# Performance work log

Measured on AMD Instinct MI355X. Metric: run time of the kernel, lower is better.

## Reference

```python
import jax, jax.numpy as jnp
import numpy as np

B, N, K, D = 4, 20000, 16, 128


def setup_inputs() -> dict:
    key = jax.random.key(0)
    k1, k2, k3, k4, k5, k6 = jax.random.split(key, 6)
    node_embeddings = jax.random.normal(k1, (B, N, D), dtype=jnp.float32)
    knn_indices = jax.random.randint(k2, (B, N, K), 0, N, dtype=jnp.int32)
    # MLP params: Linear(3D -> D), GELU, Linear(D -> D)
    s1 = 1.0 / np.sqrt(3 * D)
    s2 = 1.0 / np.sqrt(D)
    W1 = jax.random.uniform(k3, (3 * D, D), dtype=jnp.float32, minval=-s1, maxval=s1)
    b1 = jax.random.uniform(k4, (D,), dtype=jnp.float32, minval=-s1, maxval=s1)
    W2 = jax.random.uniform(k5, (D, D), dtype=jnp.float32, minval=-s2, maxval=s2)
    b2 = jax.random.uniform(k6, (D,), dtype=jnp.float32, minval=-s2, maxval=s2)
    return {"node_embeddings": node_embeddings, "knn_indices": knn_indices,
            "W1": W1, "b1": b1, "W2": W2, "b2": b2}


def reference(node_embeddings, knn_indices, W1, b1, W2, b2):
    # gather neighbors: [B, N, K, D]
    neighbors = jnp.take_along_axis(node_embeddings[:, None, :, :],  # [B,1,N,D]
                                    knn_indices[:, :, :, None].astype(jnp.int32),
                                    axis=2)
    neighbor_mean = neighbors.mean(axis=2)  # [B, N, D]
    feats = jnp.concatenate([node_embeddings, neighbor_mean,
                             node_embeddings - neighbor_mean], axis=-1)  # [B,N,3D]
    h = jax.nn.gelu(feats @ W1 + b1, approximate=False)
    update = h @ W2 + b2
    return node_embeddings + update
```

## Files before the change

kernel.cpp:

```cpp
#include <hip/hip_runtime.h>

#define NB      20000
#define BATCH   4
#define KNN     16
#define DD      128
#define MW      136
#define BMG     32
#define NSLOTG  313
#define BMF     64
#define NSLOTF  157

#define PT_ROWS   32
#define PT_TILES  625
#define WL_BYTES  98304
#define XB_BYTES  16384
#define MB_BYTES  8192
#define HB_BYTES  8192
#define PT_LDS    (WL_BYTES + 2*XB_BYTES + 2*MB_BYTES + HB_BYTES)

#if defined(__has_builtin)
#if __has_builtin(__builtin_amdgcn_cvt_pk_f32_fp8)
#define FP8_DEC_BUILTIN 1
#endif
#endif

typedef __attribute__((ext_vector_type(8))) short          bf16x8;
typedef __attribute__((ext_vector_type(4))) float          f32x4;
typedef __attribute__((ext_vector_type(2))) float          f32x2;
typedef __attribute__((ext_vector_type(4))) int            i32x4;
typedef __attribute__((ext_vector_type(2))) int            i32x2;
typedef __attribute__((ext_vector_type(4))) unsigned short u16x4;
typedef __attribute__((ext_vector_type(8))) unsigned short u16x8;

__device__ __forceinline__ unsigned short f2bf(float f) {
    unsigned int u = __float_as_uint(f);
    u += 0x7fffu + ((u >> 16) & 1u);
    return (unsigned short)(u >> 16);
}
__device__ __forceinline__ float bf2f(unsigned short u) {
    return __uint_as_float((unsigned int)u << 16);
}
__device__ __forceinline__ float gelu_fast(float z) {
    float u = z * (0.7978845608028654f + 0.0356774081f * z * z);
    float e = __expf(-2.0f * u);
    return z * __builtin_amdgcn_rcpf(1.0f + e);
}
__device__ __forceinline__ void glds16(const void* g, void* l) {
    __builtin_amdgcn_global_load_lds(
        (const __attribute__((address_space(1))) void*)g,
        (__attribute__((address_space(3))) void*)l, 16, 0, 0);
}
__device__ __forceinline__ void bar_lgkm() {
    asm volatile("s_waitcnt lgkmcnt(0)" ::: "memory");
    __builtin_amdgcn_sched_barrier(0);
    __builtin_amdgcn_s_barrier();
}
__device__ __forceinline__ void bar_full() {
    asm volatile("s_waitcnt vmcnt(0) lgkmcnt(0)" ::: "memory");
    __builtin_amdgcn_sched_barrier(0);
    __builtin_amdgcn_s_barrier();
}
__device__ __forceinline__ unsigned int f32_to_e4m3(float x) {
    unsigned int u   = __float_as_uint(x);
    unsigned int sgn = (u >> 24) & 0x80u;
    float ax = fabsf(x);
    unsigned int em;
    if (ax < 0.015625f) {
        em = (unsigned int)rintf(ax * 512.0f);
    } else {
        unsigned int mag = __float_as_uint(fminf(ax, 448.0f));
        em = ((mag + 0x7FFFFu + ((mag >> 20) & 1u)) >> 20) - 0x3C0u;
    }
    return sgn | em;
}
__device__ __forceinline__ void acc4_fp8(unsigned int w, float* s) {
#if defined(FP8_DEC_BUILTIN)
    f32x2 lo = __builtin_amdgcn_cvt_pk_f32_fp8((int)w, false);
    f32x2 hi = __builtin_amdgcn_cvt_pk_f32_fp8((int)w, true);
    s[0] += lo[0]; s[1] += lo[1]; s[2] += hi[0]; s[3] += hi[1];
#else
    #pragma unroll
    for (int j = 0; j < 4; ++j) {
        unsigned int b  = (w >> (8 * j)) & 0xFFu;
        unsigned int em = b & 0x7Fu;
        float f  = __uint_as_float((em << 20) + 0x3C000000u);
        float fd = (float)em * 0.001953125f;
        f = (em < 8u) ? fd : f;
        f = __uint_as_float(__float_as_uint(f) | ((b & 0x80u) << 24));
        s[j] += f;
    }
#endif
}
__device__ __forceinline__ u16x4 dec4_bf16(unsigned int w) {
    u16x4 o;
#if defined(FP8_DEC_BUILTIN)
    f32x2 lo = __builtin_amdgcn_cvt_pk_f32_fp8((int)w, false);
    f32x2 hi = __builtin_amdgcn_cvt_pk_f32_fp8((int)w, true);
    o[0] = f2bf(lo[0]); o[1] = f2bf(lo[1]); o[2] = f2bf(hi[0]); o[3] = f2bf(hi[1]);
#else
    #pragma unroll
    for (int j = 0; j < 4; ++j) {
        unsigned int b  = (w >> (8 * j)) & 0xFFu;
        unsigned int em = b & 0x7Fu;
        float f  = __uint_as_float((em << 20) + 0x3C000000u);
        float fd = (float)em * 0.001953125f;
        f = (em < 8u) ? fd : f;
        f = __uint_as_float(__float_as_uint(f) | ((b & 0x80u) << 24));
        o[j] = f2bf(f);
    }
#endif
    return o;
}

__device__ __forceinline__ const bf16x8* wfrag(const void* W, int col, int ko) {
    return (const bf16x8*)((const char*)W + col * 256 + (ko ^ ((col & 7) << 4)));
}

__global__ __launch_bounds__(256) void nr_prep(
    const float* __restrict__ emb, const float* __restrict__ W1,
    const float* __restrict__ W2,
    unsigned char* __restrict__ embq, unsigned short* __restrict__ Wsw)
{
    int bid = blockIdx.x;
    if (bid < 5000) {
        long long i = ((long long)bid * 256 + threadIdx.x) * 8;
        const float4* p = (const float4*)(emb + i);
        float4 a = p[0], b = p[1];
        unsigned int w0 = f32_to_e4m3(a.x) | (f32_to_e4m3(a.y) << 8) |
                          (f32_to_e4m3(a.z) << 16) | (f32_to_e4m3(a.w) << 24);
        unsigned int w1 = f32_to_e4m3(b.x) | (f32_to_e4m3(b.y) << 8) |
                          (f32_to_e4m3(b.z) << 16) | (f32_to_e4m3(b.w) << 24);
        i32x2 q; q[0] = (int)w0; q[1] = (int)w1;
        *(i32x2*)(embq + i) = q;
    } else {
        int tid = (bid - 5000) * 256 + threadIdx.x;
        int w   = tid >> 14;
        int r2  = tid & 16383;
        int col = r2 >> 7;
        int k   = r2 & 127;
        float v;
        if (w == 0)      v = W1[k * DD + col] + W1[(256 + k) * DD + col];
        else if (w == 1) v = W1[(128 + k) * DD + col] - W1[(256 + k) * DD + col];
        else             v = W2[k * DD + col];
        char* dst = (char*)Wsw + w * 32768 + col * 256 + ((k * 2) ^ ((col & 7) << 4));
        *(unsigned short*)dst = f2bf(v);
    }
}

__global__ __launch_bounds__(256, 2) void nr_gather(
    const unsigned char* __restrict__ embq, const int* __restrict__ knn,
    unsigned char* __restrict__ meanq)
{
    extern __shared__ char ldsg[];

    const int t     = threadIdx.x;
    const int xcd   = blockIdx.x & 7;
    const int slot  = blockIdx.x >> 3;
    const int batch = xcd >> 1;
    const int bib   = (xcd & 1) * NSLOTG + slot;
    const int mend  = batch * NB + NB;
    int m_base = batch * NB + bib * BMG;
    if (m_base + BMG > mend) m_base = mend - BMG;

    const int node_local = t >> 3;
    const int dpart      = t & 7;
    const int m  = m_base + node_local;
    const int wv = t >> 6;
    const int ln = t & 63;

    int idx[KNN];
    const i32x4* kp4 = (const i32x4*)(knn + (long long)m * KNN);
    #pragma unroll
    for (int q = 0; q < 4; ++q) {
        i32x4 v = __builtin_nontemporal_load(kp4 + q);
        idx[4*q+0] = v[0]; idx[4*q+1] = v[1]; idx[4*q+2] = v[2]; idx[4*q+3] = v[3];
    }

    const unsigned char* qbase = embq + (long long)batch * NB * DD + dpart * 16;
    #pragma unroll
    for (int k = 0; k < KNN; ++k)
        glds16(qbase + (long long)idx[k] * DD, ldsg + k * 4096 + wv * 1024);

    __syncthreads();

    float sm[16];
    #pragma unroll
    for (int e = 0; e < 16; ++e) sm[e] = 0.f;
    #pragma unroll
    for (int k = 0; k < KNN; ++k) {
        i32x4 v = *(const i32x4*)(ldsg + k * 4096 + wv * 1024 + ln * 16);
        acc4_fp8((unsigned int)v[0], sm + 0);
        acc4_fp8((unsigned int)v[1], sm + 4);
        acc4_fp8((unsigned int)v[2], sm + 8);
        acc4_fp8((unsigned int)v[3], sm + 12);
    }

    i32x4 o;
    #pragma unroll
    for (int j = 0; j < 4; ++j) {
        unsigned int w;
        w  = f32_to_e4m3(sm[4*j+0] * 0.0625f);
        w |= f32_to_e4m3(sm[4*j+1] * 0.0625f) << 8;
        w |= f32_to_e4m3(sm[4*j+2] * 0.0625f) << 16;
        w |= f32_to_e4m3(sm[4*j+3] * 0.0625f) << 24;
        o[j] = (int)w;
    }
    *(i32x4*)(meanq + (long long)m * DD + dpart * 16) = o;
}

__global__ __launch_bounds__(512, 2) void nr_persist(
    const float* __restrict__ emb, const unsigned char* __restrict__ meanq,
    const unsigned short* __restrict__ Wsw,
    const float* __restrict__ b1, const float* __restrict__ b2,
    float* __restrict__ out)
{
    extern __shared__ char L[];
    char* WL  = L;
    char* XB0 = L + WL_BYTES;
    char* MB0 = XB0 + 2 * XB_BYTES;
    char* HB  = MB0 + 2 * MB_BYTES;

    const int t     = threadIdx.x;
    const int xcd   = blockIdx.x & 7;
    const int bslot = blockIdx.x >> 3;
    const int batch = xcd >> 1;
    const int pair  = (xcd & 1) * 64 + bslot;
    const int wv    = t >> 6;
    const int ln    = t & 63;
    const int lrow  = ln & 15;
    const int lk    = ln >> 4;
    const int r     = wv & 1;
    const int cf0   = wv >> 1;
    const int arow  = r * 16 + lrow;
    const int xsw   = (arow & 7) << 4;

    int   colj[2]; float b1v[2], b2v[2];
    #pragma unroll
    for (int j = 0; j < 2; ++j) {
        colj[j] = (cf0 + j * 4) * 16 + lrow;
        b1v[j]  = b1[colj[j]];
        b2v[j]  = b2[colj[j]];
    }

    {
        const char* gw = (const char*)Wsw;
        #pragma unroll
        for (int i = 0; i < 12; ++i) {
            int ch = i * 8 + wv;
            glds16(gw + ch * 1024 + ln * 16, WL + ch * 1024);
        }
    }

    const long long brow = (long long)batch * NB;
    const int nt = (PT_TILES - pair + 127) >> 7;

    auto stage_x = [&](int n) {
        const long long r0 = brow + (long long)(pair + n * 128) * PT_ROWS;
        char* xb = XB0 + (n & 1) * XB_BYTES;
        const char* gx = (const char*)emb + r0 * 512;
        #pragma unroll
        for (int ci = 0; ci < 2; ++ci) {
            int ch  = wv * 2 + ci;
            int row = ch * 2 + (ln >> 5);
            int cb  = (ln & 31) * 16;
            glds16(gx + (long long)row * 512 + (cb ^ ((row & 7) << 4)),
                   xb + ch * 1024);
        }
    };
    auto load_mean = [&](int n) -> i32x2 {
        const long long r0 = brow + (long long)(pair + n * 128) * PT_ROWS;
        int row = t >> 4;
        int cb8 = (t & 15) * 8;
        return *(const i32x2*)(meanq + (r0 + row) * 128 + cb8);
    };
    auto write_mean = [&](int n, i32x2 mv) {
        char* mb = MB0 + (n & 1) * MB_BYTES;
        int row = t >> 4;
        int cb8 = (t & 15) * 8;
        u16x4 a = dec4_bf16((unsigned int)mv[0]);
        u16x4 b = dec4_bf16((unsigned int)mv[1]);
        u16x8 o;
        o[0]=a[0]; o[1]=a[1]; o[2]=a[2]; o[3]=a[3];
        o[4]=b[0]; o[5]=b[1]; o[6]=b[2]; o[7]=b[3];
        *(u16x8*)(mb + row * 256 + ((cb8 * 2) ^ ((row & 7) << 4))) = o;
    };

    stage_x(0);
    {
        i32x2 mv0 = load_mean(0);
        write_mean(0, mv0);
    }
    bar_full();

    for (int n = 0; n < nt; ++n) {
        const int p = n & 1;
        char* xb = XB0 + p * XB_BYTES;
        char* mb = MB0 + p * MB_BYTES;
        const long long r0 = brow + (long long)(pair + n * 128) * PT_ROWS;
        const bool have_next = (n + 1 < nt);

        i32x2 mv;
        if (have_next) {
            stage_x(n + 1);
            mv = load_mean(n + 1);
        }

        bf16x8 xf[4], mf[4];
        #pragma unroll
        for (int ks = 0; ks < 4; ++ks) {
            int cb = ks * 128 + lk * 32;
            f32x4 a0 = *(const f32x4*)(xb + arow * 512 + ((cb)      ^ xsw));
            f32x4 a1 = *(const f32x4*)(xb + arow * 512 + ((cb + 16) ^ xsw));
            u16x8 xt;
            xt[0]=f2bf(a0[0]); xt[1]=f2bf(a0[1]); xt[2]=f2bf(a0[2]); xt[3]=f2bf(a0[3]);
            xt[4]=f2bf(a1[0]); xt[5]=f2bf(a1[1]); xt[6]=f2bf(a1[2]); xt[7]=f2bf(a1[3]);
            xf[ks] = *(bf16x8*)&xt;
            mf[ks] = *(const bf16x8*)(mb + arow * 256 + ((ks * 64 + lk * 16) ^ xsw));
        }

        f32x4 acc[2];
        acc[0] = (f32x4){0.f,0.f,0.f,0.f}; acc[1] = (f32x4){0.f,0.f,0.f,0.f};
        #pragma unroll
        for (int ks = 0; ks < 4; ++ks)
            #pragma unroll
            for (int j = 0; j < 2; ++j) {
                bf16x8 w = *wfrag(WL, colj[j], ks * 64 + lk * 16);
                acc[j] = __builtin_amdgcn_mfma_f32_16x16x32_bf16(xf[ks], w, acc[j], 0, 0, 0);
            }
        #pragma unroll
        for (int ks = 0; ks < 4; ++ks)
            #pragma unroll
            for (int j = 0; j < 2; ++j) {
                bf16x8 w = *wfrag(WL + 32768, colj[j], ks * 64 + lk * 16);
                acc[j] = __builtin_amdgcn_mfma_f32_16x16x32_bf16(mf[ks], w, acc[j], 0, 0, 0);
            }

        #pragma unroll
        for (int j = 0; j < 2; ++j)
            #pragma unroll
            for (int rr = 0; rr < 4; ++rr) {
                int row = r * 16 + lk * 4 + rr;
                *(unsigned short*)(HB + row * 256 + ((colj[j] * 2) ^ ((row & 7) << 4)))
                    = f2bf(gelu_fast(acc[j][rr] + b1v[j]));
            }
        bar_lgkm();

        bf16x8 hf[4];
        #pragma unroll
        for (int ks = 0; ks < 4; ++ks)
            hf[ks] = *(const bf16x8*)(HB + arow * 256 + ((ks * 64 + lk * 16) ^ xsw));
        f32x4 acc2[2];
        acc2[0] = (f32x4){0.f,0.f,0.f,0.f}; acc2[1] = (f32x4){0.f,0.f,0.f,0.f};
        #pragma unroll
        for (int ks = 0; ks < 4; ++ks)
            #pragma unroll
            for (int j = 0; j < 2; ++j) {
                bf16x8 w = *wfrag(WL + 65536, colj[j], ks * 64 + lk * 16);
                acc2[j] = __builtin_amdgcn_mfma_f32_16x16x32_bf16(hf[ks], w, acc2[j], 0, 0, 0);
            }

        if (have_next) write_mean(n + 1, mv);

        #pragma unroll
        for (int j = 0; j < 2; ++j)
            #pragma unroll
            for (int rr = 0; rr < 4; ++rr) {
                int row = r * 16 + lk * 4 + rr;
                int col = colj[j];
                float xv = *(const float*)(xb + row * 512 + ((col * 4) ^ ((row & 7) << 4)));
                out[(r0 + row) * 128 + col] = acc2[j][rr] + b2v[j] + xv;
            }
        bar_full();
    }
}

template<int MODE>
__global__ __launch_bounds__(256, 3) void nr_fused(
    const float* __restrict__ emb, const unsigned char* __restrict__ meanq,
    const int* __restrict__ knn, const unsigned short* __restrict__ Wsw,
    const float* __restrict__ b1, const float* __restrict__ b2,
    float* __restrict__ out)
{
    extern __shared__ char ldsraw[];
    float*          ldsxF = (float*)ldsraw;
    unsigned short* ldsm  = (unsigned short*)(ldsraw + BMF * DD * 4);

    const int t     = threadIdx.x;
    const int xcd   = blockIdx.x & 7;
    const int slot  = blockIdx.x >> 3;
    const int batch = xcd >> 1;
    const int bib   = (xcd & 1) * NSLOTF + slot;
    const int mend  = batch * NB + NB;
    int m_base = batch * NB + bib * BMF;
    if (m_base + BMF > mend) m_base = mend - BMF;

    {
        const int node_local = t >> 2;
        const int dpart      = t & 3;
        const int m  = m_base + node_local;
        const int wv = t >> 6;
        const int ln = t & 63;

        if constexpr (MODE == 0) {
            const i32x4* mp = (const i32x4*)(meanq + (long long)m * DD + dpart * 32);
            i32x4 v0 = mp[0], v1 = mp[1];
            const char* gx = (const char*)(emb + (long long)m_base * DD);
            #pragma unroll
            for (int it = 0; it < 8; ++it) {
                int off = it * 4096 + wv * 1024;
                glds16(gx + off + ln * 16, ldsraw + off);
            }
            unsigned short* mrow = ldsm + node_local * MW + dpart * 32;
            #pragma unroll
            for (int j = 0; j < 4; ++j) {
                *(u16x4*)(mrow + j*4)      = dec4_bf16((unsigned int)v0[j]);
                *(u16x4*)(mrow + 16 + j*4) = dec4_bf16((unsigned int)v1[j]);
            }
        } else {
            const f32x4* xp = (const f32x4*)(emb + (long long)m * DD + dpart * 32);
            float* xrow = ldsxF + node_local * DD + dpart * 32;
            #pragma unroll
            for (int j = 0; j < 8; ++j) {
                f32x4 v = xp[j];
                *(f32x4*)(xrow + j*4) = v;
            }
            int idx[KNN];
            const i32x4* kp4 = (const i32x4*)(knn + (long long)m * KNN);
            #pragma unroll
            for (int q = 0; q < 4; ++q) {
                i32x4 v = __builtin_nontemporal_load(kp4 + q);
                idx[4*q+0]=v[0]; idx[4*q+1]=v[1]; idx[4*q+2]=v[2]; idx[4*q+3]=v[3];
            }
            float sm[32];
            #pragma unroll
            for (int e = 0; e < 32; ++e) sm[e] = 0.f;
            const long long bbase = (long long)batch * NB * DD + dpart * 32;
            #pragma unroll 4
            for (int k = 0; k < KNN; ++k) {
                const f32x4* np = (const f32x4*)(emb + bbase + (long long)idx[k] * DD);
                #pragma unroll
                for (int j = 0; j < 8; ++j) {
                    f32x4 v = np[j];
                    sm[j*4+0]+=v[0]; sm[j*4+1]+=v[1]; sm[j*4+2]+=v[2]; sm[j*4+3]+=v[3];
                }
            }
            unsigned short* mrow = ldsm + node_local * MW + dpart * 32;
            #pragma unroll
            for (int j = 0; j < 8; ++j) {
                u16x4 pm;
                #pragma unroll
                for (int e = 0; e < 4; ++e) pm[e] = f2bf(sm[j*4+e] * 0.0625f);
                *(u16x4*)(mrow + j*4) = pm;
            }
        }
    }
    __syncthreads();

    const int wave = t >> 6;
    const int lane = t & 63;
    const int lrow = lane & 15;
    const int lk   = lane >> 4;
    const int Arow = wave * 16 + lrow;

    bf16x8 xf[4], mf[4];
    {
        const float* xr = ldsxF + Arow * DD + lk * 8;
        const unsigned short* mr = ldsm + Arow * MW + lk * 8;
        #pragma unroll
        for (int ks = 0; ks < 4; ++ks) {
            f32x4 a0 = *(const f32x4*)(xr + ks * 32);
            f32x4 a1 = *(const f32x4*)(xr + ks * 32 + 4);
            u16x8 xt;
            xt[0]=f2bf(a0[0]); xt[1]=f2bf(a0[1]); xt[2]=f2bf(a0[2]); xt[3]=f2bf(a0[3]);
            xt[4]=f2bf(a1[0]); xt[5]=f2bf(a1[1]); xt[6]=f2bf(a1[2]); xt[7]=f2bf(a1[3]);
            xf[ks] = *(bf16x8*)&xt;
            mf[ks] = *(const bf16x8*)(mr + ks * 32);
        }
    }

    f32x4 acc[8];
    #pragma unroll
    for (int f = 0; f < 8; ++f) acc[f] = (f32x4){0.f, 0.f, 0.f, 0.f};
    #pragma unroll
    for (int ks = 0; ks < 4; ++ks)
        #pragma unroll
        for (int f = 0; f < 8; ++f) {
            bf16x8 bw = *wfrag(Wsw, f * 16 + lrow, ks * 64 + lk * 16);
            acc[f] = __builtin_amdgcn_mfma_f32_16x16x32_bf16(xf[ks], bw, acc[f], 0, 0, 0);
        }
    #pragma unroll
    for (int ks = 0; ks < 4; ++ks)
        #pragma unroll
        for (int f = 0; f < 8; ++f) {
            bf16x8 bw = *wfrag((const char*)Wsw + 32768, f * 16 + lrow, ks * 64 + lk * 16);
            acc[f] = __builtin_amdgcn_mfma_f32_16x16x32_bf16(mf[ks], bw, acc[f], 0, 0, 0);
        }
    __syncthreads();

    #pragma unroll
    for (int f = 0; f < 8; ++f) {
        int col = f * 16 + lrow;
        float bb = b1[col];
        #pragma unroll
        for (int rr = 0; rr < 4; ++rr) {
            int row = wave * 16 + lk * 4 + rr;
            ldsm[row * MW + col] = f2bf(gelu_fast(acc[f][rr] + bb));
        }
    }
    __syncthreads();

    f32x4 acc2[8];
    #pragma unroll
    for (int f = 0; f < 8; ++f) acc2[f] = (f32x4){0.f, 0.f, 0.f, 0.f};
    {
        const unsigned short* abase = ldsm + Arow * MW + lk * 8;
        #pragma unroll
        for (int ks = 0; ks < 4; ++ks) {
            bf16x8 af = *(const bf16x8*)(abase + ks * 32);
            #pragma unroll
            for (int f = 0; f < 8; ++f) {
                bf16x8 bw = *wfrag((const char*)Wsw + 65536, f * 16 + lrow, ks * 64 + lk * 16);
                acc2[f] = __builtin_amdgcn_mfma_f32_16x16x32_bf16(af, bw, acc2[f], 0, 0, 0);
            }
        }
    }

    #pragma unroll
    for (int f = 0; f < 8; ++f) {
        int col = f * 16 + lrow;
        float bb = b2[col];
        #pragma unroll
        for (int rr = 0; rr < 4; ++rr) {
            int row = wave * 16 + lk * 4 + rr;
            float xv = ldsxF[row * DD + col];
            out[(long long)(m_base + row) * DD + col] = acc2[f][rr] + bb + xv;
        }
    }
}

extern "C" void kernel_launch(void* const* d_in, const int* in_sizes, int n_in,
                              void* d_out, int out_size, void* d_ws, size_t ws_size,
                              hipStream_t stream) {
    const float* emb = (const float*)d_in[0];
    const int*   knn = (const int*)  d_in[1];
    const float* W1  = (const float*)d_in[2];
    const float* b1  = (const float*)d_in[3];
    const float* W2  = (const float*)d_in[4];
    const float* b2  = (const float*)d_in[5];
    float* out = (float*)d_out;

    unsigned short* Wsw   = (unsigned short*)d_ws;
    unsigned char*  embq  = (unsigned char*)(Wsw + 49152);
    unsigned char*  meanq = embq + 10240000;

    const size_t NEED   = (size_t)98304 + 10240000 + 10240000;
    const size_t LDSB_F = (size_t)BMF * DD * 4 + (size_t)BMF * MW * 2;

    if (ws_size >= NEED) {
        hipError_t e = hipFuncSetAttribute(
            reinterpret_cast<const void*>(nr_persist),
            hipFuncAttributeMaxDynamicSharedMemorySize, PT_LDS);
        nr_prep<<<5192, 256, 0, stream>>>(emb, W1, W2, embq, Wsw);
        nr_gather<<<8 * NSLOTG, 256, 65536, stream>>>(embq, knn, meanq);
        if (e == hipSuccess) {
            nr_persist<<<512, 512, PT_LDS, stream>>>(
                emb, meanq, Wsw, b1, b2, out);
        } else {
            nr_fused<0><<<8 * NSLOTF, 256, LDSB_F, stream>>>(
                emb, meanq, knn, Wsw, b1, b2, out);
        }
    } else {
        nr_prep<<<5192, 256, 0, stream>>>(emb, W1, W2, embq, Wsw);
        nr_fused<2><<<8 * NSLOTF, 256, LDSB_F, stream>>>(
            emb, nullptr, knn, Wsw, b1, b2, out);
    }
}
```

Before: 63.71 us.

## Hold weight fragments in registers and halve persistent grid in nr_persist

Moves the three bf16 weight matrices out of LDS into per-thread register fragments loaded once, and loads fp8 mean values straight from global into registers instead of staging them through LDS. LDS use per block drops to the x staging buffers plus the hidden buffer, and the persistent grid goes from 512 to 256 blocks, each handling twice as many tiles. This removes the repeated LDS weight reads in the MFMA loops and the mean staging writes. The cost is higher register pressure from 48 bf16x8 fragments plus prefetched means, which could spill or limit occupancy, and fewer blocks to hide latency. The fallback path is also cleaned up so it no longer needs meanq, and prep skips the emb quantization there.

```diff
diff --git a/kernel.cpp b/kernel.cpp
--- a/kernel.cpp
+++ b/kernel.cpp
@@ -12,11 +12,9 @@
 
 #define PT_ROWS   32
 #define PT_TILES  625
-#define WL_BYTES  98304
 #define XB_BYTES  16384
-#define MB_BYTES  8192
 #define HB_BYTES  8192
-#define PT_LDS    (WL_BYTES + 2*XB_BYTES + 2*MB_BYTES + HB_BYTES)
+#define PT_LDS    (2*XB_BYTES + HB_BYTES)
 
 #if defined(__has_builtin)
 #if __has_builtin(__builtin_amdgcn_cvt_pk_f32_fp8)
@@ -116,13 +114,14 @@
     return (const bf16x8*)((const char*)W + col * 256 + (ko ^ ((col & 7) << 4)));
 }
 
+template<bool DO_EMB>
 __global__ __launch_bounds__(256) void nr_prep(
     const float* __restrict__ emb, const float* __restrict__ W1,
     const float* __restrict__ W2,
     unsigned char* __restrict__ embq, unsigned short* __restrict__ Wsw)
 {
     int bid = blockIdx.x;
-    if (bid < 5000) {
+    if (DO_EMB && bid < 5000) {
         long long i = ((long long)bid * 256 + threadIdx.x) * 8;
         const float4* p = (const float4*)(emb + i);
         float4 a = p[0], b = p[1];
@@ -133,7 +132,7 @@
         i32x2 q; q[0] = (int)w0; q[1] = (int)w1;
         *(i32x2*)(embq + i) = q;
     } else {
-        int tid = (bid - 5000) * 256 + threadIdx.x;
+        int tid = (bid - (DO_EMB ? 5000 : 0)) * 256 + threadIdx.x;
         int w   = tid >> 14;
         int r2  = tid & 16383;
         int col = r2 >> 7;
@@ -215,16 +214,14 @@
     float* __restrict__ out)
 {
     extern __shared__ char L[];
-    char* WL  = L;
-    char* XB0 = L + WL_BYTES;
-    char* MB0 = XB0 + 2 * XB_BYTES;
-    char* HB  = MB0 + 2 * MB_BYTES;
+    char* XB0 = L;
+    char* HB  = L + 2 * XB_BYTES;
 
     const int t     = threadIdx.x;
     const int xcd   = blockIdx.x & 7;
     const int bslot = blockIdx.x >> 3;
     const int batch = xcd >> 1;
-    const int pair  = (xcd & 1) * 64 + bslot;
+    const int pair  = (xcd & 1) * 32 + bslot;
     const int wv    = t >> 6;
     const int ln    = t & 63;
     const int lrow  = ln & 15;
@@ -242,20 +239,22 @@
         b2v[j]  = b2[colj[j]];
     }
 
-    {
-        const char* gw = (const char*)Wsw;
-        #pragma unroll
-        for (int i = 0; i < 12; ++i) {
-            int ch = i * 8 + wv;
-            glds16(gw + ch * 1024 + ln * 16, WL + ch * 1024);
-        }
-    }
+    bf16x8 wA[4][2], wB[4][2], wC[4][2];
+    #pragma unroll
+    for (int ks = 0; ks < 4; ++ks)
+        #pragma unroll
+        for (int j = 0; j < 2; ++j) {
+            int ko = ks * 64 + lk * 16;
+            wA[ks][j] = *wfrag(Wsw, colj[j], ko);
+            wB[ks][j] = *wfrag((const char*)Wsw + 32768, colj[j], ko);
+            wC[ks][j] = *wfrag((const char*)Wsw + 65536, colj[j], ko);
+        }
 
     const long long brow = (long long)batch * NB;
-    const int nt = (PT_TILES - pair + 127) >> 7;
+    const int nt = (PT_TILES - pair + 63) >> 6;
 
     auto stage_x = [&](int n) {
-        const long long r0 = brow + (long long)(pair + n * 128) * PT_ROWS;
+        const long long r0 = brow + (long long)(pair + n * 64) * PT_ROWS;
         char* xb = XB0 + (n & 1) * XB_BYTES;
         const char* gx = (const char*)emb + r0 * 512;
         #pragma unroll
@@ -267,42 +266,28 @@
                    xb + ch * 1024);
         }
     };
-    auto load_mean = [&](int n) -> i32x2 {
-        const long long r0 = brow + (long long)(pair + n * 128) * PT_ROWS;
-        int row = t >> 4;
-        int cb8 = (t & 15) * 8;
-        return *(const i32x2*)(meanq + (r0 + row) * 128 + cb8);
+    auto load_mean = [&](int n, i32x2* mv) {
+        const long long r0 = brow + (long long)(pair + n * 64) * PT_ROWS;
+        const unsigned char* mq = meanq + (r0 + arow) * 128 + lk * 8;
+        #pragma unroll
+        for (int ks = 0; ks < 4; ++ks)
+            mv[ks] = *(const i32x2*)(mq + ks * 32);
     };
-    auto write_mean = [&](int n, i32x2 mv) {
-        char* mb = MB0 + (n & 1) * MB_BYTES;
-        int row = t >> 4;
-        int cb8 = (t & 15) * 8;
-        u16x4 a = dec4_bf16((unsigned int)mv[0]);
-        u16x4 b = dec4_bf16((unsigned int)mv[1]);
-        u16x8 o;
-        o[0]=a[0]; o[1]=a[1]; o[2]=a[2]; o[3]=a[3];
-        o[4]=b[0]; o[5]=b[1]; o[6]=b[2]; o[7]=b[3];
-        *(u16x8*)(mb + row * 256 + ((cb8 * 2) ^ ((row & 7) << 4))) = o;
-    };
-
+
+    i32x2 mv_cur[4], mv_nxt[4];
     stage_x(0);
-    {
-        i32x2 mv0 = load_mean(0);
-        write_mean(0, mv0);
-    }
+    load_mean(0, mv_cur);
     bar_full();
 
     for (int n = 0; n < nt; ++n) {
         const int p = n & 1;
         char* xb = XB0 + p * XB_BYTES;
-        char* mb = MB0 + p * MB_BYTES;
-        const long long r0 = brow + (long long)(pair + n * 128) * PT_ROWS;
+        const long long r0 = brow + (long long)(pair + n * 64) * PT_ROWS;
         const bool have_next = (n + 1 < nt);
 
-        i32x2 mv;
         if (have_next) {
             stage_x(n + 1);
-            mv = load_mean(n + 1);
+            load_mean(n + 1, mv_nxt);
         }
 
         bf16x8 xf[4], mf[4];
@@ -315,7 +300,12 @@
             xt[0]=f2bf(a0[0]); xt[1]=f2bf(a0[1]); xt[2]=f2bf(a0[2]); xt[3]=f2bf(a0[3]);
             xt[4]=f2bf(a1[0]); xt[5]=f2bf(a1[1]); xt[6]=f2bf(a1[2]); xt[7]=f2bf(a1[3]);
             xf[ks] = *(bf16x8*)&xt;
-            mf[ks] = *(const bf16x8*)(mb + arow * 256 + ((ks * 64 + lk * 16) ^ xsw));
+            u16x4 mlo = dec4_bf16((unsigned int)mv_cur[ks][0]);
+            u16x4 mhi = dec4_bf16((unsigned int)mv_cur[ks][1]);
+            u16x8 mt;
+            mt[0]=mlo[0]; mt[1]=mlo[1]; mt[2]=mlo[2]; mt[3]=mlo[3];
+            mt[4]=mhi[0]; mt[5]=mhi[1]; mt[6]=mhi[2]; mt[7]=mhi[3];
+            mf[ks] = *(bf16x8*)&mt;
         }
 
         f32x4 acc[2];
@@ -323,17 +313,13 @@
         #pragma unroll
         for (int ks = 0; ks < 4; ++ks)
             #pragma unroll
-            for (int j = 0; j < 2; ++j) {
-                bf16x8 w = *wfrag(WL, colj[j], ks * 64 + lk * 16);
-                acc[j] = __builtin_amdgcn_mfma_f32_16x16x32_bf16(xf[ks], w, acc[j], 0, 0, 0);
-            }
+            for (int j = 0; j < 2; ++j)
+                acc[j] = __builtin_amdgcn_mfma_f32_16x16x32_bf16(xf[ks], wA[ks][j], acc[j], 0, 0, 0);
         #pragma unroll
         for (int ks = 0; ks < 4; ++ks)
             #pragma unroll
-            for (int j = 0; j < 2; ++j) {
-                bf16x8 w = *wfrag(WL + 32768, colj[j], ks * 64 + lk * 16);
-                acc[j] = __builtin_amdgcn_mfma_f32_16x16x32_bf16(mf[ks], w, acc[j], 0, 0, 0);
-            }
+            for (int j = 0; j < 2; ++j)
+                acc[j] = __builtin_amdgcn_mfma_f32_16x16x32_bf16(mf[ks], wB[ks][j], acc[j], 0, 0, 0);
 
         #pragma unroll
         for (int j = 0; j < 2; ++j)
@@ -354,12 +340,8 @@
         #pragma unroll
         for (int ks = 0; ks < 4; ++ks)
             #pragma unroll
-            for (int j = 0; j < 2; ++j) {
-                bf16x8 w = *wfrag(WL + 65536, colj[j], ks * 64 + lk * 16);
-                acc2[j] = __builtin_amdgcn_mfma_f32_16x16x32_bf16(hf[ks], w, acc2[j], 0, 0, 0);
-            }
-
-        if (have_next) write_mean(n + 1, mv);
+            for (int j = 0; j < 2; ++j)
+                acc2[j] = __builtin_amdgcn_mfma_f32_16x16x32_bf16(hf[ks], wC[ks][j], acc2[j], 0, 0, 0);
 
         #pragma unroll
         for (int j = 0; j < 2; ++j)
@@ -370,14 +352,18 @@
                 float xv = *(const float*)(xb + row * 512 + ((col * 4) ^ ((row & 7) << 4)));
                 out[(r0 + row) * 128 + col] = acc2[j][rr] + b2v[j] + xv;
             }
+
+        if (have_next) {
+            #pragma unroll
+            for (int ks = 0; ks < 4; ++ks) mv_cur[ks] = mv_nxt[ks];
+        }
         bar_full();
     }
 }
 
-template<int MODE>
-__global__ __launch_bounds__(256, 3) void nr_fused(
-    const float* __restrict__ emb, const unsigned char* __restrict__ meanq,
-    const int* __restrict__ knn, const unsigned short* __restrict__ Wsw,
+__global__ __launch_bounds__(256, 3) void nr_fused_f32(
+    const float* __restrict__ emb, const int* __restrict__ knn,
+    const unsigned short* __restrict__ Wsw,
     const float* __restrict__ b1, const float* __restrict__ b2,
     float* __restrict__ out)
 {
@@ -398,60 +384,41 @@
         const int node_local = t >> 2;
         const int dpart      = t & 3;
         const int m  = m_base + node_local;
-        const int wv = t >> 6;
-        const int ln = t & 63;
-
-        if constexpr (MODE == 0) {
-            const i32x4* mp = (const i32x4*)(meanq + (long long)m * DD + dpart * 32);
-            i32x4 v0 = mp[0], v1 = mp[1];
-            const char* gx = (const char*)(emb + (long long)m_base * DD);
-            #pragma unroll
-            for (int it = 0; it < 8; ++it) {
-                int off = it * 4096 + wv * 1024;
-                glds16(gx + off + ln * 16, ldsraw + off);
+
+        const f32x4* xp = (const f32x4*)(emb + (long long)m * DD + dpart * 32);
+        float* xrow = ldsxF + node_local * DD + dpart * 32;
+        #pragma unroll
+        for (int j = 0; j < 8; ++j) {
+            f32x4 v = xp[j];
+            *(f32x4*)(xrow + j*4) = v;
+        }
+        int idx[KNN];
+        const i32x4* kp4 = (const i32x4*)(knn + (long long)m * KNN);
+        #pragma unroll
+        for (int q = 0; q < 4; ++q) {
+            i32x4 v = __builtin_nontemporal_load(kp4 + q);
+            idx[4*q+0]=v[0]; idx[4*q+1]=v[1]; idx[4*q+2]=v[2]; idx[4*q+3]=v[3];
+        }
+        float sm[32];
+        #pragma unroll
+        for (int e = 0; e < 32; ++e) sm[e] = 0.f;
+        const long long bbase = (long long)batch * NB * DD + dpart * 32;
+        #pragma unroll 4
+        for (int k = 0; k < KNN; ++k) {
+            const f32x4* np = (const f32x4*)(emb + bbase + (long long)idx[k] * DD);
+            #pragma unroll
+            for (int j = 0; j < 8; ++j) {
+                f32x4 v = np[j];
+                sm[j*4+0]+=v[0]; sm[j*4+1]+=v[1]; sm[j*4+2]+=v[2]; sm[j*4+3]+=v[3];
             }
-            unsigned short* mrow = ldsm + node_local * MW + dpart * 32;
-            #pragma unroll
-            for (int j = 0; j < 4; ++j) {
-                *(u16x4*)(mrow + j*4)      = dec4_bf16((unsigned int)v0[j]);
-                *(u16x4*)(mrow + 16 + j*4) = dec4_bf16((unsigned int)v1[j]);
-            }
-        } else {
-            const f32x4* xp = (const f32x4*)(emb + (long long)m * DD + dpart * 32);
-            float* xrow = ldsxF + node_local * DD + dpart * 32;
-            #pragma unroll
-            for (int j = 0; j < 8; ++j) {
-                f32x4 v = xp[j];
-                *(f32x4*)(xrow + j*4) = v;
-            }
-            int idx[KNN];
-            const i32x4* kp4 = (const i32x4*)(knn + (long long)m * KNN);
-            #pragma unroll
-            for (int q = 0; q < 4; ++q) {
-                i32x4 v = __builtin_nontemporal_load(kp4 + q);
-                idx[4*q+0]=v[0]; idx[4*q+1]=v[1]; idx[4*q+2]=v[2]; idx[4*q+3]=v[3];
-            }
-            float sm[32];
-            #pragma unroll
-            for (int e = 0; e < 32; ++e) sm[e] = 0.f;
-            const long long bbase = (long long)batch * NB * DD + dpart * 32;
-            #pragma unroll 4
-            for (int k = 0; k < KNN; ++k) {
-                const f32x4* np = (const f32x4*)(emb + bbase + (long long)idx[k] * DD);
-                #pragma unroll
-                for (int j = 0; j < 8; ++j) {
-                    f32x4 v = np[j];
-                    sm[j*4+0]+=v[0]; sm[j*4+1]+=v[1]; sm[j*4+2]+=v[2]; sm[j*4+3]+=v[3];
-                }
-            }
-            unsigned short* mrow = ldsm + node_local * MW + dpart * 32;
-            #pragma unroll
-            for (int j = 0; j < 8; ++j) {
-                u16x4 pm;
-                #pragma unroll
-                for (int e = 0; e < 4; ++e) pm[e] = f2bf(sm[j*4+e] * 0.0625f);
-                *(u16x4*)(mrow + j*4) = pm;
-            }
+        }
+        unsigned short* mrow = ldsm + node_local * MW + dpart * 32;
+        #pragma unroll
+        for (int j = 0; j < 8; ++j) {
+            u16x4 pm;
+            #pragma unroll
+            for (int e = 0; e < 4; ++e) pm[e] = f2bf(sm[j*4+e] * 0.0625f);
+            *(u16x4*)(mrow + j*4) = pm;
         }
     }
     __syncthreads();
@@ -557,21 +524,12 @@
     const size_t LDSB_F = (size_t)BMF * DD * 4 + (size_t)BMF * MW * 2;
 
     if (ws_size >= NEED) {
-        hipError_t e = hipFuncSetAttribute(
-            reinterpret_cast<const void*>(nr_persist),
-            hipFuncAttributeMaxDynamicSharedMemorySize, PT_LDS);
-        nr_prep<<<5192, 256, 0, stream>>>(emb, W1, W2, embq, Wsw);
+        nr_prep<true><<<5192, 256, 0, stream>>>(emb, W1, W2, embq, Wsw);
         nr_gather<<<8 * NSLOTG, 256, 65536, stream>>>(embq, knn, meanq);
-        if (e == hipSuccess) {
-            nr_persist<<<512, 512, PT_LDS, stream>>>(
-                emb, meanq, Wsw, b1, b2, out);
-        } else {
-            nr_fused<0><<<8 * NSLOTF, 256, LDSB_F, stream>>>(
-                emb, meanq, knn, Wsw, b1, b2, out);
-        }
+        nr_persist<<<256, 512, PT_LDS, stream>>>(emb, meanq, Wsw, b1, b2, out);
     } else {
-        nr_prep<<<5192, 256, 0, stream>>>(emb, W1, W2, embq, Wsw);
-        nr_fused<2><<<8 * NSLOTF, 256, LDSB_F, stream>>>(
-            emb, nullptr, knn, Wsw, b1, b2, out);
-    }
-}
+        nr_prep<false><<<192, 256, 0, stream>>>(emb, W1, W2, nullptr, Wsw);
+        nr_fused_f32<<<8 * NSLOTF, 256, LDSB_F, stream>>>(
+            emb, knn, Wsw, b1, b2, out);
+    }
+}
```

New measurement: 66.26 us. 4.0% more time.
